# Performance work log

Measured on AMD Instinct MI355X. Metric: run time of the kernel, lower is better.

The kernel has to match this reference:

```python
import jax, jax.numpy as jnp
import numpy as np

N = 50000
E = 1600000
IN = 128
HID = 128
OUT = 64
NEG_SLOPE = 0.2  # DGL GATConv default leaky_relu slope


def _gat_layer(h, src, dst, W, al, ar, b, res=None, act=True):
    """DGL GATConv layer on an edge-list graph.
    h: [N, F_in]; W: [F_in, H*D]; al, ar, b: [H, D]; res: None | [N,H,D].
    Returns [N, H, D].
    """
    H, D = al.shape
    f = (h @ W).reshape(N, H, D)                      # fc projection
    el = jnp.sum(f * al, axis=-1)                     # [N, H]
    er = jnp.sum(f * ar, axis=-1)                     # [N, H]
    e = jax.nn.leaky_relu(el[src] + er[dst], NEG_SLOPE)  # [E, H]
    # edge softmax over incoming edges of each dst node
    m = jax.ops.segment_max(e, dst, num_segments=N)   # [N, H]
    ex = jnp.exp(e - m[dst])                          # [E, H]
    s = jax.ops.segment_sum(ex, dst, num_segments=N)  # [N, H]
    alpha = ex / s[dst]                               # [E, H]
    msg = f[src] * alpha[..., None]                   # [E, H, D]
    rst = jax.ops.segment_sum(msg, dst, num_segments=N)  # [N, H, D]
    if res is not None:
        rst = rst + res
    rst = rst + b                                     # bias [H, D] broadcast
    if act:
        rst = jax.nn.elu(rst)
    return rst


def setup_inputs() -> dict:
    key = jax.random.key(0)
    ks = jax.random.split(key, 16)
    x = jax.random.normal(ks[0], (N, IN), dtype=jnp.float32)
    src = jax.random.randint(ks[1], (E,), 0, N)
    dst = jax.random.randint(ks[2], (E,), 0, N)
    sc = 0.05
    # layer 0: IN -> 8 heads x 16, no residual, elu
    W0 = jax.random.normal(ks[3], (IN, 8 * 16), dtype=jnp.float32) * sc
    al0 = jax.random.normal(ks[4], (8, 16), dtype=jnp.float32) * sc
    ar0 = jax.random.normal(ks[5], (8, 16), dtype=jnp.float32) * sc
    b0 = jnp.zeros((8, 16), dtype=jnp.float32)
    # layer 1: HID -> 8 heads x 16, identity residual (HID == 8*16), elu
    W1 = jax.random.normal(ks[6], (HID, 8 * 16), dtype=jnp.float32) * sc
    al1 = jax.random.normal(ks[7], (8, 16), dtype=jnp.float32) * sc
    ar1 = jax.random.normal(ks[8], (8, 16), dtype=jnp.float32) * sc
    b1 = jnp.zeros((8, 16), dtype=jnp.float32)
    # layer 2: HID -> 1 head x 64, linear residual (128 != 64), no act
    W2 = jax.random.normal(ks[9], (HID, 1 * OUT), dtype=jnp.float32) * sc
    al2 = jax.random.normal(ks[10], (1, OUT), dtype=jnp.float32) * sc
    ar2 = jax.random.normal(ks[11], (1, OUT), dtype=jnp.float32) * sc
    b2 = jnp.zeros((1, OUT), dtype=jnp.float32)
    resW2 = jax.random.normal(ks[12], (HID, 1 * OUT), dtype=jnp.float32) * sc
    return {"x": x, "src": src, "dst": dst,
            "W0": W0, "al0": al0, "ar0": ar0, "b0": b0,
            "W1": W1, "al1": al1, "ar1": ar1, "b1": b1,
            "W2": W2, "al2": al2, "ar2": ar2, "b2": b2,
            "resW2": resW2}


def reference(x, src, dst, W0, al0, ar0, b0, W1, al1, ar1, b1,
              W2, al2, ar2, b2, resW2):
    # layer 0: no residual, elu, flatten heads (dropout=0)
    h = _gat_layer(x, src, dst, W0, al0, ar0, b0, res=None, act=True)
    h = h.reshape(N, -1)  # [N, 128]
    # layer 1: identity residual, elu, flatten heads
    res1 = h.reshape(N, 8, 16)
    h = _gat_layer(h, src, dst, W1, al1, ar1, b1, res=res1, act=True)
    h = h.reshape(N, -1)  # [N, 128]
    # layer 2: linear residual, no activation, mean over heads
    res2 = (h @ resW2).reshape(N, 1, OUT)
    h = _gat_layer(h, src, dst, W2, al2, ar2, b2, res=res2, act=False)
    return h.mean(axis=1)  # [N, 64]
```

## Files before the change

### kernel.cpp

```cpp
#include <hip/hip_runtime.h>
#include <hip/hip_fp16.h>
#include <math.h>


#define GN 50000
#define GE 1600000
#define NB 391
#define NBLK_A 512
#define CHUNK 3125
#define NBD 200
#define DCH 250

typedef _Float16 half8 __attribute__((ext_vector_type(8)));
typedef _Float16 half4v __attribute__((ext_vector_type(4)));
typedef float f32x4 __attribute__((ext_vector_type(4)));


__global__ __launch_bounds__(256) void bucketA(const int* __restrict__ dst, int* __restrict__ cnt) {
    __shared__ int hist[NB];
    for (int i = threadIdx.x; i < NB; i += 256) hist[i] = 0;
    __syncthreads();
    int b = blockIdx.x;
    int beg = b * CHUNK, end = beg + CHUNK;
    for (int i = beg + threadIdx.x; i < end; i += 256)
        atomicAdd(&hist[dst[i] >> 7], 1);
    __syncthreads();
    for (int k = threadIdx.x; k < NB; k += 256)
        cnt[k * NBLK_A + b] = hist[k];
}

__global__ __launch_bounds__(512) void bucketB(int* __restrict__ cnt, int* __restrict__ tot) {
    __shared__ int s[512];
    int k = blockIdx.x, t = threadIdx.x;
    int* row = cnt + k * NBLK_A;
    s[t] = row[t];
    __syncthreads();
    for (int ofs = 1; ofs < 512; ofs <<= 1) {
        int v = (t >= ofs) ? s[t - ofs] : 0;
        __syncthreads();
        s[t] += v;
        __syncthreads();
    }
    row[t] = (t == 0) ? 0 : s[t - 1];
    if (t == 511) tot[k] = s[511];
}

__global__ __launch_bounds__(512) void bucketB2(const int* __restrict__ tot, int* __restrict__ base,
                                                int* __restrict__ offs) {
    __shared__ int s[512];
    int t = threadIdx.x;
    s[t] = (t < NB) ? tot[t] : 0;
    __syncthreads();
    for (int ofs = 1; ofs < 512; ofs <<= 1) {
        int v = (t >= ofs) ? s[t - ofs] : 0;
        __syncthreads();
        s[t] += v;
        __syncthreads();
    }
    if (t <= NB) base[t] = (t == 0) ? 0 : s[t - 1];
    if (t == 0) offs[GN] = GE;
}

__global__ __launch_bounds__(256) void bucketC(const int* __restrict__ src, const int* __restrict__ dst,
                                               const int* __restrict__ cnt, const int* __restrict__ base,
                                               unsigned* __restrict__ ebuf) {
    __shared__ int cur[NB];
    int b = blockIdx.x;
    for (int k = threadIdx.x; k < NB; k += 256)
        cur[k] = base[k] + cnt[k * NBLK_A + b];
    __syncthreads();
    int beg = b * CHUNK, end = beg + CHUNK;
    for (int i = beg + threadIdx.x; i < end; i += 256) {
        int d = dst[i];
        int pos = atomicAdd(&cur[d >> 7], 1);
        ebuf[pos] = (unsigned)src[i] | ((unsigned)(d & 127) << 16);
    }
}

__global__ __launch_bounds__(256) void bucketD(const unsigned* __restrict__ ebuf, const int* __restrict__ base,
                                               int* __restrict__ offs, int* __restrict__ csrc) {
    __shared__ int hist[4096];
    __shared__ int psum[256];
    int k = blockIdx.x, t = threadIdx.x;
    #pragma unroll
    for (int i = 0; i < 16; ++i) hist[t * 16 + i] = 0;
    __syncthreads();
    int lo = base[k], hi = base[k + 1];
    for (int i = lo + t; i < hi; i += 256) {
        unsigned v = ebuf[i];
        unsigned key = ((v >> 16) << 5) | ((v & 0xFFFFu) >> 11);
        atomicAdd(&hist[key], 1);
    }
    __syncthreads();
    int loc[16];
    int s = 0;
    #pragma unroll
    for (int i = 0; i < 16; ++i) { loc[i] = s; s += hist[t * 16 + i]; }
    psum[t] = s;
    __syncthreads();
    for (int ofs = 1; ofs < 256; ofs <<= 1) {
        int v = (t >= ofs) ? psum[t - ofs] : 0;
        __syncthreads();
        psum[t] += v;
        __syncthreads();
    }
    int basek = lo + ((t == 0) ? 0 : psum[t - 1]);
    #pragma unroll
    for (int i = 0; i < 16; ++i) hist[t * 16 + i] = basek + loc[i];
    __syncthreads();
    if (t < 128) {
        int node = (k << 7) + t;
        if (node < GN) offs[node] = hist[t * 32];
    }
    __syncthreads();
    for (int i = lo + t; i < hi; i += 256) {
        unsigned v = ebuf[i];
        unsigned key = ((v >> 16) << 5) | ((v & 0xFFFFu) >> 11);
        int pos = atomicAdd(&hist[key], 1);
        csrc[pos] = (int)(v & 0xFFFFu);
    }
}


__global__ __launch_bounds__(256) void dhist(const int* __restrict__ offs, int* __restrict__ dcnt) {
    __shared__ int hist[128];
    int b = blockIdx.x, t = threadIdx.x;
    if (t < 128) hist[t] = 0;
    __syncthreads();
    int n = b * DCH + t;
    if (t < DCH && n < GN) {
        int d = offs[n + 1] - offs[n];
        d = (d > 127) ? 127 : d;
        atomicAdd(&hist[d], 1);
    }
    __syncthreads();
    if (t < 128) dcnt[t * NBD + b] = hist[t];
}

__global__ __launch_bounds__(256) void dscanB(int* __restrict__ dcnt, int* __restrict__ dtot) {
    __shared__ int s[256];
    int k = blockIdx.x, t = threadIdx.x;
    int* row = dcnt + k * NBD;
    s[t] = (t < NBD) ? row[t] : 0;
    __syncthreads();
    for (int ofs = 1; ofs < 256; ofs <<= 1) {
        int v = (t >= ofs) ? s[t - ofs] : 0;
        __syncthreads();
        s[t] += v;
        __syncthreads();
    }
    if (t < NBD) row[t] = (t == 0) ? 0 : s[t - 1];
    if (t == 255) dtot[k] = s[255];
}

__global__ __launch_bounds__(128) void dscanB2(const int* __restrict__ dtot, int* __restrict__ dbase) {
    __shared__ int s[128];
    int t = threadIdx.x;
    s[t] = dtot[t];
    __syncthreads();
    for (int ofs = 1; ofs < 128; ofs <<= 1) {
        int v = (t >= ofs) ? s[t - ofs] : 0;
        __syncthreads();
        s[t] += v;
        __syncthreads();
    }
    dbase[t] = (t == 0) ? 0 : s[t - 1];
}

__global__ __launch_bounds__(256) void dscat(const int* __restrict__ offs, const int* __restrict__ dcnt,
                                             const int* __restrict__ dbase, int* __restrict__ perm) {
    __shared__ int cur[128];
    int b = blockIdx.x, t = threadIdx.x;
    if (t < 128) cur[t] = dbase[t] + dcnt[t * NBD + b];
    __syncthreads();
    int n = b * DCH + t;
    if (t < DCH && n < GN) {
        int d = offs[n + 1] - offs[n];
        d = (d > 127) ? 127 : d;
        int pos = atomicAdd(&cur[d], 1);
        perm[pos] = n;
    }
}


__global__ __launch_bounds__(256) void prep(const float* __restrict__ W0, const float* __restrict__ W1,
                                            const float* __restrict__ W2, const float* __restrict__ rW2,
                                            const float* __restrict__ al0, const float* __restrict__ ar0,
                                            const float* __restrict__ al1, const float* __restrict__ ar1,
                                            const float* __restrict__ al2, const float* __restrict__ ar2,
                                            _Float16* __restrict__ w0t, _Float16* __restrict__ w1t,
                                            _Float16* __restrict__ w2t, _Float16* __restrict__ rw2t,
                                            _Float16* __restrict__ aB0, _Float16* __restrict__ aB1,
                                            _Float16* __restrict__ aB2) {
    int i = blockIdx.x * 256 + threadIdx.x;
    if (i < 16384) {
        int n = i >> 7, k = i & 127;
        w0t[i] = (_Float16)W0[k * 128 + n];
        w1t[i] = (_Float16)W1[k * 128 + n];
    }
    if (i < 8192) {
        int n = i >> 7, k = i & 127;
        w2t[i] = (_Float16)W2[k * 64 + n];
        rw2t[i] = (_Float16)rW2[k * 64 + n];
    }
    if (i < 2048) {
        int n = i >> 7, k = i & 127;
        _Float16 v0 = (_Float16)0.f, v1 = (_Float16)0.f, v2 = (_Float16)0.f;
        if (n < 8) {
            if ((k >> 4) == n) {
                v0 = (_Float16)al0[n * 16 + (k & 15)];
                v1 = (_Float16)al1[n * 16 + (k & 15)];
            }
        } else {
            int h = n - 8;
            if ((k >> 4) == h) {
                v0 = (_Float16)ar0[h * 16 + (k & 15)];
                v1 = (_Float16)ar1[h * 16 + (k & 15)];
            }
        }
        if (n == 0 && k < 64) v2 = (_Float16)al2[k];
        if (n == 1 && k < 64) v2 = (_Float16)ar2[k];
        aB0[i] = v0; aB1[i] = v1; aB2[i] = v2;
    }
}


template <int NT, bool AF32, bool DUAL, bool MULTI>
__global__ __launch_bounds__(256) void gemm_att(const void* __restrict__ Av,
                                                const _Float16* __restrict__ WT,
                                                const _Float16* __restrict__ WT2,
                                                const _Float16* __restrict__ attB,
                                                _Float16* __restrict__ C, _Float16* __restrict__ C2,
                                                float* __restrict__ elb, float* __restrict__ erb,
                                                int nrows) {
    const int N = NT * 16;
    __shared__ _Float16 lt[4][16][NT * 16 + 4];
    int wave = threadIdx.x >> 6, lane = threadIdx.x & 63;
    int quad = lane >> 4, l16 = lane & 15;
    int m = blockIdx.x * 64 + wave * 16 + l16;
    int mc = (m < nrows) ? m : (nrows - 1);
    half8 a[4];
    if (AF32) {
        const float* ap = (const float*)Av + (size_t)mc * 128 + quad * 8;
        #pragma unroll
        for (int kk = 0; kk < 4; ++kk) {
            float4 u = *(const float4*)(ap + kk * 32);
            float4 v = *(const float4*)(ap + kk * 32 + 4);
            half8 t;
            t[0] = (_Float16)u.x; t[1] = (_Float16)u.y; t[2] = (_Float16)u.z; t[3] = (_Float16)u.w;
            t[4] = (_Float16)v.x; t[5] = (_Float16)v.y; t[6] = (_Float16)v.z; t[7] = (_Float16)v.w;
            a[kk] = t;
        }
    } else {
        const _Float16* ap = (const _Float16*)Av + (size_t)mc * 128 + quad * 8;
        #pragma unroll
        for (int kk = 0; kk < 4; ++kk) a[kk] = *(const half8*)(ap + kk * 32);
    }
    f32x4 acc[NT];
    f32x4 acc2[DUAL ? NT : 1];
    #pragma unroll
    for (int nt = 0; nt < NT; ++nt) acc[nt] = (f32x4){0.f, 0.f, 0.f, 0.f};
    if (DUAL) {
        #pragma unroll
        for (int nt = 0; nt < NT; ++nt) acc2[nt] = (f32x4){0.f, 0.f, 0.f, 0.f};
    }
    const _Float16* wp = WT + (size_t)l16 * 128 + quad * 8;
    const _Float16* wp2 = DUAL ? (WT2 + (size_t)l16 * 128 + quad * 8) : WT;
    #pragma unroll
    for (int nt = 0; nt < NT; ++nt) {
        #pragma unroll
        for (int kk = 0; kk < 4; ++kk) {
            half8 b = *(const half8*)(wp + nt * 16 * 128 + kk * 32);
            acc[nt] = __builtin_amdgcn_mfma_f32_16x16x32_f16(a[kk], b, acc[nt], 0, 0, 0);
            if (DUAL) {
                half8 b2 = *(const half8*)(wp2 + nt * 16 * 128 + kk * 32);
                acc2[nt] = __builtin_amdgcn_mfma_f32_16x16x32_f16(a[kk], b2, acc2[nt], 0, 0, 0);
            }
        }
    }
    int row0 = blockIdx.x * 64 + wave * 16 + quad * 4;
    #pragma unroll
    for (int nt = 0; nt < NT; ++nt) {
        #pragma unroll
        for (int r = 0; r < 4; ++r) {
            _Float16 hv = (_Float16)acc[nt][r];
            lt[wave][quad * 4 + r][nt * 16 + l16] = hv;
            int row = row0 + r;
            if (row < nrows) {
                C[(size_t)row * N + nt * 16 + l16] = hv;
                if (DUAL) C2[(size_t)row * N + nt * 16 + l16] = (_Float16)acc2[nt][r];
            }
        }
    }
    f32x4 att = {0.f, 0.f, 0.f, 0.f};
    const _Float16* bp = attB + (size_t)l16 * 128 + quad * 8;
    constexpr int KCH = (NT == 8) ? 4 : 2;
    #pragma unroll
    for (int kk = 0; kk < KCH; ++kk) {
        const _Float16* lp = &lt[wave][l16][kk * 32 + quad * 8];
        half4v lo = *(const half4v*)lp;
        half4v hi = *(const half4v*)(lp + 4);
        half8 af = __builtin_shufflevector(lo, hi, 0, 1, 2, 3, 4, 5, 6, 7);
        half8 bf = *(const half8*)(bp + kk * 32);
        att = __builtin_amdgcn_mfma_f32_16x16x32_f16(af, bf, att, 0, 0, 0);
    }
    if (MULTI) {
        int hh = l16 & 7;
        float* dstp = (l16 < 8) ? elb : erb;
        #pragma unroll
        for (int r = 0; r < 4; ++r) {
            int row = row0 + r;
            if (row < nrows) dstp[row * 8 + hh] = att[r];
        }
    } else {
        if (l16 < 2) {
            float* dstp = (l16 == 0) ? elb : erb;
            #pragma unroll
            for (int r = 0; r < 4; ++r) {
                int row = row0 + r;
                if (row < nrows) dstp[row] = att[r];
            }
        }
    }
}


__global__ __launch_bounds__(256) void agg_multi(const int* __restrict__ offs, const int* __restrict__ csrc,
                                                 const int* __restrict__ perm,
                                                 const _Float16* __restrict__ fh, const float* __restrict__ el,
                                                 const float* __restrict__ er, const float* __restrict__ bias,
                                                 const _Float16* __restrict__ resid, _Float16* __restrict__ out,
                                                 int n) {
    int slot = blockIdx.x * 16 + (threadIdx.x >> 4);
    int lg = threadIdx.x & 15;
    if (slot >= n) return;
    int node = perm[n - 1 - slot];
    int head = lg >> 1;
    float ern = er[node * 8 + head];
    int beg = offs[node], end = offs[node + 1];
    float acc[8] = {};
    float ssum = 0.f;
    int e = beg;
    for (; e + 4 <= end; e += 4) {
        int s0 = csrc[e], s1 = csrc[e + 1], s2 = csrc[e + 2], s3 = csrc[e + 3];
        float e0 = el[s0 * 8 + head] + ern;
        float e1 = el[s1 * 8 + head] + ern;
        float e2 = el[s2 * 8 + head] + ern;
        float e3 = el[s3 * 8 + head] + ern;
        half8 q0 = *(const half8*)(fh + (size_t)s0 * 128 + lg * 8);
        half8 q1 = *(const half8*)(fh + (size_t)s1 * 128 + lg * 8);
        half8 q2 = *(const half8*)(fh + (size_t)s2 * 128 + lg * 8);
        half8 q3 = *(const half8*)(fh + (size_t)s3 * 128 + lg * 8);
        e0 = fmaxf(e0, 0.2f * e0);
        e1 = fmaxf(e1, 0.2f * e1);
        e2 = fmaxf(e2, 0.2f * e2);
        e3 = fmaxf(e3, 0.2f * e3);
        float w0 = __expf(e0), w1 = __expf(e1), w2 = __expf(e2), w3 = __expf(e3);
        ssum += (w0 + w1) + (w2 + w3);
        #pragma unroll
        for (int i = 0; i < 8; ++i)
            acc[i] += w0 * (float)q0[i] + w1 * (float)q1[i]
                    + w2 * (float)q2[i] + w3 * (float)q3[i];
    }
    for (; e < end; ++e) {
        int s = csrc[e];
        float ev = el[s * 8 + head] + ern;
        ev = fmaxf(ev, 0.2f * ev);
        float w = __expf(ev);
        half8 q = *(const half8*)(fh + (size_t)s * 128 + lg * 8);
        ssum += w;
        #pragma unroll
        for (int i = 0; i < 8; ++i) acc[i] += w * (float)q[i];
    }
    float inv = (ssum > 0.f) ? 1.0f / ssum : 0.f;
    float o[8];
    #pragma unroll
    for (int j = 0; j < 8; ++j) o[j] = acc[j] * inv + bias[lg * 8 + j];
    if (resid) {
        half8 r = *(const half8*)(resid + (size_t)node * 128 + lg * 8);
        #pragma unroll
        for (int j = 0; j < 8; ++j) o[j] += (float)r[j];
    }
    half8 ov;
    #pragma unroll
    for (int j = 0; j < 8; ++j) {
        float v = o[j];
        v = (v > 0.f) ? v : expm1f(v);
        ov[j] = (_Float16)v;
    }
    *(half8*)(out + (size_t)node * 128 + lg * 8) = ov;
}

__global__ __launch_bounds__(256) void agg_single(const int* __restrict__ offs, const int* __restrict__ csrc,
                                                  const int* __restrict__ perm,
                                                  const _Float16* __restrict__ fh, const float* __restrict__ el,
                                                  const float* __restrict__ er, const float* __restrict__ bias,
                                                  const _Float16* __restrict__ resid, float* __restrict__ out,
                                                  int n) {
    int slot = blockIdx.x * 16 + (threadIdx.x >> 4);
    int lg = threadIdx.x & 15;
    if (slot >= n) return;
    int node = perm[n - 1 - slot];
    float ern = er[node];
    int beg = offs[node], end = offs[node + 1];
    float acc[4] = {};
    float ssum = 0.f;
    int e = beg;
    for (; e + 4 <= end; e += 4) {
        int s0 = csrc[e], s1 = csrc[e + 1], s2 = csrc[e + 2], s3 = csrc[e + 3];
        float e0 = el[s0] + ern;
        float e1 = el[s1] + ern;
        float e2 = el[s2] + ern;
        float e3 = el[s3] + ern;
        half4v q0 = *(const half4v*)(fh + (size_t)s0 * 64 + lg * 4);
        half4v q1 = *(const half4v*)(fh + (size_t)s1 * 64 + lg * 4);
        half4v q2 = *(const half4v*)(fh + (size_t)s2 * 64 + lg * 4);
        half4v q3 = *(const half4v*)(fh + (size_t)s3 * 64 + lg * 4);
        e0 = fmaxf(e0, 0.2f * e0);
        e1 = fmaxf(e1, 0.2f * e1);
        e2 = fmaxf(e2, 0.2f * e2);
        e3 = fmaxf(e3, 0.2f * e3);
        float w0 = __expf(e0), w1 = __expf(e1), w2 = __expf(e2), w3 = __expf(e3);
        ssum += (w0 + w1) + (w2 + w3);
        #pragma unroll
        for (int i = 0; i < 4; ++i)
            acc[i] += w0 * (float)q0[i] + w1 * (float)q1[i]
                    + w2 * (float)q2[i] + w3 * (float)q3[i];
    }
    for (; e < end; ++e) {
        int s = csrc[e];
        float ev = el[s] + ern;
        ev = fmaxf(ev, 0.2f * ev);
        float w = __expf(ev);
        half4v q = *(const half4v*)(fh + (size_t)s * 64 + lg * 4);
        ssum += w;
        #pragma unroll
        for (int i = 0; i < 4; ++i) acc[i] += w * (float)q[i];
    }
    float inv = (ssum > 0.f) ? 1.0f / ssum : 0.f;
    half4v r = *(const half4v*)(resid + (size_t)node * 64 + lg * 4);
    float4 o;
    o.x = acc[0] * inv + bias[lg * 4 + 0] + (float)r[0];
    o.y = acc[1] * inv + bias[lg * 4 + 1] + (float)r[1];
    o.z = acc[2] * inv + bias[lg * 4 + 2] + (float)r[2];
    o.w = acc[3] * inv + bias[lg * 4 + 3] + (float)r[3];
    *(float4*)(out + (size_t)node * 64 + lg * 4) = o;
}


extern "C" void kernel_launch(void* const* d_in, const int* in_sizes, int n_in,
                              void* d_out, int out_size, void* d_ws, size_t ws_size,
                              hipStream_t stream) {
    const float* x     = (const float*)d_in[0];
    const int*   src   = (const int*)d_in[1];
    const int*   dst   = (const int*)d_in[2];
    const float* W0    = (const float*)d_in[3];
    const float* al0   = (const float*)d_in[4];
    const float* ar0   = (const float*)d_in[5];
    const float* b0    = (const float*)d_in[6];
    const float* W1    = (const float*)d_in[7];
    const float* al1   = (const float*)d_in[8];
    const float* ar1   = (const float*)d_in[9];
    const float* b1    = (const float*)d_in[10];
    const float* W2    = (const float*)d_in[11];
    const float* al2   = (const float*)d_in[12];
    const float* ar2   = (const float*)d_in[13];
    const float* b2    = (const float*)d_in[14];
    const float* resW2 = (const float*)d_in[15];
    float* out = (float*)d_out;

    char* w = (char*)d_ws;
    auto alloc = [&](size_t bytes) {
        char* p = w;
        w += (bytes + 255) & ~(size_t)255;
        return p;
    };
    int*      base  = (int*)alloc((size_t)(NB + 1) * 4);
    int*      offs  = (int*)alloc((size_t)(GN + 1) * 4);
    int*      csrc  = (int*)alloc((size_t)GE * 4);
    int*      perm  = (int*)alloc((size_t)GN * 4);
    int*      dcnt  = (int*)alloc((size_t)128 * NBD * 4);
    int*      dtot  = (int*)alloc(128 * 4);
    int*      dbase = (int*)alloc(128 * 4);
    _Float16* fbuf  = (_Float16*)alloc((size_t)GN * 128 * 2);
    float*    elb   = (float*)alloc((size_t)GN * 8 * 4);
    float*    erb   = (float*)alloc((size_t)GN * 8 * 4);
    _Float16* hA    = (_Float16*)alloc((size_t)GN * 128 * 2);
    _Float16* hB    = (_Float16*)alloc((size_t)GN * 128 * 2);
    _Float16* res2  = (_Float16*)alloc((size_t)GN * 64 * 2);
    _Float16* w0t   = (_Float16*)alloc(128 * 128 * 2);
    _Float16* w1t   = (_Float16*)alloc(128 * 128 * 2);
    _Float16* w2t   = (_Float16*)alloc(64 * 128 * 2);
    _Float16* rw2t  = (_Float16*)alloc(64 * 128 * 2);
    _Float16* aB0   = (_Float16*)alloc(16 * 128 * 2);
    _Float16* aB1   = (_Float16*)alloc(16 * 128 * 2);
    _Float16* aB2   = (_Float16*)alloc(16 * 128 * 2);

    int*      cnt  = (int*)hA;
    int*      tot  = (int*)hA + NB * NBLK_A;
    unsigned* ebuf = (unsigned*)hB;

    bucketA<<<NBLK_A, 256, 0, stream>>>(dst, cnt);
    bucketB<<<NB, 512, 0, stream>>>(cnt, tot);
    bucketB2<<<1, 512, 0, stream>>>(tot, base, offs);
    bucketC<<<NBLK_A, 256, 0, stream>>>(src, dst, cnt, base, ebuf);
    bucketD<<<NB, 256, 0, stream>>>(ebuf, base, offs, csrc);

    dhist<<<NBD, 256, 0, stream>>>(offs, dcnt);
    dscanB<<<128, 256, 0, stream>>>(dcnt, dtot);
    dscanB2<<<1, 128, 0, stream>>>(dtot, dbase);
    dscat<<<NBD, 256, 0, stream>>>(offs, dcnt, dbase, perm);

    prep<<<64, 256, 0, stream>>>(W0, W1, W2, resW2, al0, ar0, al1, ar1, al2, ar2,
                                 w0t, w1t, w2t, rw2t, aB0, aB1, aB2);

    dim3 gblk(256);
    int gemmGrid = (GN + 63) / 64;
    int aggGrid = (GN + 15) / 16;

    gemm_att<8, true, false, true><<<gemmGrid, gblk, 0, stream>>>(
        x, w0t, nullptr, aB0, fbuf, nullptr, elb, erb, GN);
    agg_multi<<<aggGrid, gblk, 0, stream>>>(offs, csrc, perm, fbuf, elb, erb, b0, nullptr, hA, GN);

    gemm_att<8, false, false, true><<<gemmGrid, gblk, 0, stream>>>(
        hA, w1t, nullptr, aB1, fbuf, nullptr, elb, erb, GN);
    agg_multi<<<aggGrid, gblk, 0, stream>>>(offs, csrc, perm, fbuf, elb, erb, b1, hA, hB, GN);

    gemm_att<4, false, true, false><<<gemmGrid, gblk, 0, stream>>>(
        hB, w2t, rw2t, aB2, fbuf, res2, elb, erb, GN);
    agg_single<<<aggGrid, gblk, 0, stream>>>(offs, csrc, perm, fbuf, elb, erb, b2, res2, out, GN);
}
```

Baseline: 366.1 us.

## Split aggregation by feature slice so head-slice gathers stay in cache

The aggregation kernels now give each thread group only a 32-column slice of a node's features, and blocks are interleaved so consecutive blocks cover neighbouring nodes with different slices. Each group is 8 lanes with 4 halves each instead of 16 lanes with 8 halves. The intent is to shrink the working set of gathered source rows per slice so they fit better in L2 or MALL and the random gathers hit cache more often. In exchange, edge indices, el values and the softmax exponentials are recomputed once per slice (4x for multi-head, 2x for single), and each gather is a narrower 8-byte access.

```diff
diff --git a/kernel.cpp b/kernel.cpp
--- a/kernel.cpp
+++ b/kernel.cpp
@@ -331,14 +331,19 @@
                                                  const float* __restrict__ er, const float* __restrict__ bias,
                                                  const _Float16* __restrict__ resid, _Float16* __restrict__ out,
                                                  int n) {
-    int slot = blockIdx.x * 16 + (threadIdx.x >> 4);
-    int lg = threadIdx.x & 15;
+    int b = blockIdx.x;
+    int hp = (b & 7) >> 1;
+    int nb = (b >> 3) * 2 + (b & 1);
+    int g = threadIdx.x >> 3;
+    int lane = threadIdx.x & 7;
+    int slot = nb * 32 + g;
     if (slot >= n) return;
     int node = perm[n - 1 - slot];
-    int head = lg >> 1;
+    int head = hp * 2 + (lane >> 2);
+    int col = hp * 32 + lane * 4;
     float ern = er[node * 8 + head];
     int beg = offs[node], end = offs[node + 1];
-    float acc[8] = {};
+    float acc[4] = {};
     float ssum = 0.f;
     int e = beg;
     for (; e + 4 <= end; e += 4) {
@@ -347,10 +352,10 @@
         float e1 = el[s1 * 8 + head] + ern;
         float e2 = el[s2 * 8 + head] + ern;
         float e3 = el[s3 * 8 + head] + ern;
-        half8 q0 = *(const half8*)(fh + (size_t)s0 * 128 + lg * 8);
-        half8 q1 = *(const half8*)(fh + (size_t)s1 * 128 + lg * 8);
-        half8 q2 = *(const half8*)(fh + (size_t)s2 * 128 + lg * 8);
-        half8 q3 = *(const half8*)(fh + (size_t)s3 * 128 + lg * 8);
+        half4v q0 = *(const half4v*)(fh + (size_t)s0 * 128 + col);
+        half4v q1 = *(const half4v*)(fh + (size_t)s1 * 128 + col);
+        half4v q2 = *(const half4v*)(fh + (size_t)s2 * 128 + col);
+        half4v q3 = *(const half4v*)(fh + (size_t)s3 * 128 + col);
         e0 = fmaxf(e0, 0.2f * e0);
         e1 = fmaxf(e1, 0.2f * e1);
         e2 = fmaxf(e2, 0.2f * e2);
@@ -358,7 +363,7 @@
         float w0 = __expf(e0), w1 = __expf(e1), w2 = __expf(e2), w3 = __expf(e3);
         ssum += (w0 + w1) + (w2 + w3);
         #pragma unroll
-        for (int i = 0; i < 8; ++i)
+        for (int i = 0; i < 4; ++i)
             acc[i] += w0 * (float)q0[i] + w1 * (float)q1[i]
                     + w2 * (float)q2[i] + w3 * (float)q3[i];
     }
@@ -367,28 +372,28 @@
         float ev = el[s * 8 + head] + ern;
         ev = fmaxf(ev, 0.2f * ev);
         float w = __expf(ev);
-        half8 q = *(const half8*)(fh + (size_t)s * 128 + lg * 8);
+        half4v q = *(const half4v*)(fh + (size_t)s * 128 + col);
         ssum += w;
         #pragma unroll
-        for (int i = 0; i < 8; ++i) acc[i] += w * (float)q[i];
+        for (int i = 0; i < 4; ++i) acc[i] += w * (float)q[i];
     }
     float inv = (ssum > 0.f) ? 1.0f / ssum : 0.f;
-    float o[8];
-    #pragma unroll
-    for (int j = 0; j < 8; ++j) o[j] = acc[j] * inv + bias[lg * 8 + j];
+    float o[4];
+    #pragma unroll
+    for (int j = 0; j < 4; ++j) o[j] = acc[j] * inv + bias[col + j];
     if (resid) {
-        half8 r = *(const half8*)(resid + (size_t)node * 128 + lg * 8);
-        #pragma unroll
-        for (int j = 0; j < 8; ++j) o[j] += (float)r[j];
-    }
-    half8 ov;
-    #pragma unroll
-    for (int j = 0; j < 8; ++j) {
+        half4v r = *(const half4v*)(resid + (size_t)node * 128 + col);
+        #pragma unroll
+        for (int j = 0; j < 4; ++j) o[j] += (float)r[j];
+    }
+    half4v ov;
+    #pragma unroll
+    for (int j = 0; j < 4; ++j) {
         float v = o[j];
         v = (v > 0.f) ? v : expm1f(v);
         ov[j] = (_Float16)v;
     }
-    *(half8*)(out + (size_t)node * 128 + lg * 8) = ov;
+    *(half4v*)(out + (size_t)node * 128 + col) = ov;
 }
 
 __global__ __launch_bounds__(256) void agg_single(const int* __restrict__ offs, const int* __restrict__ csrc,
@@ -397,10 +402,15 @@
                                                   const float* __restrict__ er, const float* __restrict__ bias,
                                                   const _Float16* __restrict__ resid, float* __restrict__ out,
                                                   int n) {
-    int slot = blockIdx.x * 16 + (threadIdx.x >> 4);
-    int lg = threadIdx.x & 15;
+    int b = blockIdx.x;
+    int hf = (b & 7) >> 2;
+    int nb = (b >> 3) * 4 + (b & 3);
+    int g = threadIdx.x >> 3;
+    int lane = threadIdx.x & 7;
+    int slot = nb * 32 + g;
     if (slot >= n) return;
     int node = perm[n - 1 - slot];
+    int col = hf * 32 + lane * 4;
     float ern = er[node];
     int beg = offs[node], end = offs[node + 1];
     float acc[4] = {};
@@ -412,10 +422,10 @@
         float e1 = el[s1] + ern;
         float e2 = el[s2] + ern;
         float e3 = el[s3] + ern;
-        half4v q0 = *(const half4v*)(fh + (size_t)s0 * 64 + lg * 4);
-        half4v q1 = *(const half4v*)(fh + (size_t)s1 * 64 + lg * 4);
-        half4v q2 = *(const half4v*)(fh + (size_t)s2 * 64 + lg * 4);
-        half4v q3 = *(const half4v*)(fh + (size_t)s3 * 64 + lg * 4);
+        half4v q0 = *(const half4v*)(fh + (size_t)s0 * 64 + col);
+        half4v q1 = *(const half4v*)(fh + (size_t)s1 * 64 + col);
+        half4v q2 = *(const half4v*)(fh + (size_t)s2 * 64 + col);
+        half4v q3 = *(const half4v*)(fh + (size_t)s3 * 64 + col);
         e0 = fmaxf(e0, 0.2f * e0);
         e1 = fmaxf(e1, 0.2f * e1);
         e2 = fmaxf(e2, 0.2f * e2);
@@ -432,19 +442,19 @@
         float ev = el[s] + ern;
         ev = fmaxf(ev, 0.2f * ev);
         float w = __expf(ev);
-        half4v q = *(const half4v*)(fh + (size_t)s * 64 + lg * 4);
+        half4v q = *(const half4v*)(fh + (size_t)s * 64 + col);
         ssum += w;
         #pragma unroll
         for (int i = 0; i < 4; ++i) acc[i] += w * (float)q[i];
     }
     float inv = (ssum > 0.f) ? 1.0f / ssum : 0.f;
-    half4v r = *(const half4v*)(resid + (size_t)node * 64 + lg * 4);
+    half4v r = *(const half4v*)(resid + (size_t)node * 64 + col);
     float4 o;
-    o.x = acc[0] * inv + bias[lg * 4 + 0] + (float)r[0];
-    o.y = acc[1] * inv + bias[lg * 4 + 1] + (float)r[1];
-    o.z = acc[2] * inv + bias[lg * 4 + 2] + (float)r[2];
-    o.w = acc[3] * inv + bias[lg * 4 + 3] + (float)r[3];
-    *(float4*)(out + (size_t)node * 64 + lg * 4) = o;
+    o.x = acc[0] * inv + bias[col + 0] + (float)r[0];
+    o.y = acc[1] * inv + bias[col + 1] + (float)r[1];
+    o.z = acc[2] * inv + bias[col + 2] + (float)r[2];
+    o.w = acc[3] * inv + bias[col + 3] + (float)r[3];
+    *(float4*)(out + (size_t)node * 64 + col) = o;
 }
 
 
@@ -516,17 +526,19 @@
 
     dim3 gblk(256);
     int gemmGrid = (GN + 63) / 64;
-    int aggGrid = (GN + 15) / 16;
+    int nb32 = (GN + 31) / 32;
+    int gridM = 8 * ((nb32 + 1) / 2);
+    int gridS = 8 * ((nb32 + 3) / 4);
 
     gemm_att<8, true, false, true><<<gemmGrid, gblk, 0, stream>>>(
         x, w0t, nullptr, aB0, fbuf, nullptr, elb, erb, GN);
-    agg_multi<<<aggGrid, gblk, 0, stream>>>(offs, csrc, perm, fbuf, elb, erb, b0, nullptr, hA, GN);
+    agg_multi<<<gridM, gblk, 0, stream>>>(offs, csrc, perm, fbuf, elb, erb, b0, nullptr, hA, GN);
 
     gemm_att<8, false, false, true><<<gemmGrid, gblk, 0, stream>>>(
         hA, w1t, nullptr, aB1, fbuf, nullptr, elb, erb, GN);
-    agg_multi<<<aggGrid, gblk, 0, stream>>>(offs, csrc, perm, fbuf, elb, erb, b1, hA, hB, GN);
+    agg_multi<<<gridM, gblk, 0, stream>>>(offs, csrc, perm, fbuf, elb, erb, b1, hA, hB, GN);
 
     gemm_att<4, false, true, false><<<gemmGrid, gblk, 0, stream>>>(
         hB, w2t, rw2t, aB2, fbuf, res2, elb, erb, GN);
-    agg_single<<<aggGrid, gblk, 0, stream>>>(offs, csrc, perm, fbuf, elb, erb, b2, res2, out, GN);
-}
+    agg_single<<<gridS, gblk, 0, stream>>>(offs, csrc, perm, fbuf, elb, erb, b2, res2, out, GN);
+}
```

New measurement: 505.8 us. +38.2%, slower.
